# Performance work log

Hardware: AMD Instinct MI355X
Metric: run time of the kernel (lower is better)

Reference implementation:

```python
import jax, jax.numpy as jnp
import numpy as np

B, S, D, H = 2, 2048, 1024, 16
DK = D // H  # 64
ROPE_THETA = 10000.0


def apply_rope(t, positions):
    # t: [B, H, S, DK]; positions: [B, S]
    half = DK // 2
    inv_freq = 1.0 / (ROPE_THETA ** (jnp.arange(0, DK, 2, dtype=jnp.float32) / DK))  # [half]
    ang = positions.astype(jnp.float32)[:, None, :, None] * inv_freq  # [B,1,S,half]
    cos, sin = jnp.cos(ang), jnp.sin(ang)
    t_even = t[..., 0::2]
    t_odd = t[..., 1::2]
    r_even = t_even * cos - t_odd * sin
    r_odd = t_even * sin + t_odd * cos
    # interleave back to original layout
    return jnp.stack([r_even, r_odd], axis=-1).reshape(t.shape)


def setup_inputs() -> dict:
    key = jax.random.key(0)
    ks = jax.random.split(key, 5)
    x = jax.random.normal(ks[0], (B, S, D), dtype=jnp.float32)
    token_positions = jnp.broadcast_to(jnp.arange(S, dtype=jnp.int64 if jax.config.jax_enable_x64 else jnp.int32), (B, S))
    w_q = jax.random.normal(ks[1], (D, D), dtype=jnp.float32)
    w_k = jax.random.normal(ks[2], (D, D), dtype=jnp.float32)
    w_v = jax.random.normal(ks[3], (D, D), dtype=jnp.float32)
    w_o = jax.random.normal(ks[4], (D, D), dtype=jnp.float32)
    return {"x": x, "token_positions": token_positions, "w_q": w_q, "w_k": w_k, "w_v": w_v, "w_o": w_o}


def reference(x, token_positions, w_q, w_k, w_v, w_o):
    # project: weights stored as (h*d_k, d_model)
    wq = w_q.reshape(H, DK, D)
    wk = w_k.reshape(H, DK, D)
    wv = w_v.reshape(H, DK, D)
    q = jnp.einsum('bsd,hkd->bhsk', x, wq)  # [B,H,S,DK]
    k = jnp.einsum('bsd,hkd->bhsk', x, wk)
    v = jnp.einsum('bsd,hkd->bhsk', x, wv)
    q = apply_rope(q, token_positions)
    k = apply_rope(k, token_positions)
    scale = 1.0 / jnp.sqrt(jnp.float32(DK))
    scores = jnp.einsum('bhnk,bhmk->bhnm', q, k) * scale  # [B,H,S,S]
    causal = jnp.tril(jnp.ones((S, S), dtype=bool))
    scores = jnp.where(causal, scores, -jnp.inf)
    attn = jax.nn.softmax(scores, axis=-1)
    out = jnp.einsum('bhnm,bhmv->bhnv', attn, v)  # [B,H,S,DK]
    out = jnp.transpose(out, (0, 2, 1, 3)).reshape(B, S, H * DK)
    return jnp.einsum('bsf,df->bsd', out, w_o)
```

## Files before the change

### kernel.cpp

```cpp
#include <hip/hip_runtime.h>

typedef unsigned short u16;
typedef unsigned int u32;
typedef __attribute__((ext_vector_type(8))) __bf16 bf16x8;
typedef __attribute__((ext_vector_type(4))) float f32x4;

#define NSEQ 2048
#define NDIM 1024
#define NHEAD 16
#define NTOK 4096
#define NX   4194304
#define NWEL 1048576

__device__ __forceinline__ u16 f2bf(float f) {
  unsigned u = __float_as_uint(f);
  return (u16)((u + 0x7fffu + ((u >> 16) & 1u)) >> 16);
}
__device__ __forceinline__ float bf2f(u16 h) {
  return __uint_as_float(((unsigned)h) << 16);
}
__device__ __forceinline__ bf16x8 ld16(const u16* p) {
  int4 v = *reinterpret_cast<const int4*>(p);
  return __builtin_bit_cast(bf16x8, v);
}
__device__ __forceinline__ f32x4 mfma16(bf16x8 a, bf16x8 b, f32x4 c) {
  return __builtin_amdgcn_mfma_f32_16x16x32_bf16(a, b, c, 0, 0, 0);
}
__device__ __forceinline__ u32 cvtpk(float lo, float hi) {
  u32 r;
  asm("v_cvt_pk_bf16_f32 %0, %1, %2" : "=v"(r) : "v"(lo), "v"(hi));
  return r;
}
__device__ __forceinline__ void gload16(const u16* g, u16* l) {
  __builtin_amdgcn_global_load_lds(
      (const __attribute__((address_space(1))) void*)g,
      (__attribute__((address_space(3))) void*)l, 16, 0, 0);
}

#define GEMM_PROLOGUE                                                         \
  const int tid = threadIdx.x;                                                \
  const int lane = tid & 63, wid = tid >> 6;                                  \
  const int wm = wid >> 1, wn = wid & 1;                                      \
  const int lr = lane & 15, lg = lane >> 4;                                   \
  const int srow_ = tid >> 2;                                                 \
  const int sch_ = ((tid & 3) ^ ((tid >> 3) & 3)) * 8;                        \
  const int rsw_ = (lg ^ ((lr >> 1) & 3)) * 8;

#define STAGE3(BB, AH, AL, BH, BL, T0, J0, K0)                                \
  {                                                                           \
    u16* bb_ = (BB);                                                          \
    gload16(AH + (size_t)((T0) + srow_) * NDIM + (K0) + sch_, bb_ + tid * 8); \
    gload16(AH + (size_t)((T0) + 64 + srow_) * NDIM + (K0) + sch_,            \
            bb_ + 2048 + tid * 8);                                            \
    gload16(BH + (size_t)((J0) + srow_) * NDIM + (K0) + sch_,                 \
            bb_ + 4096 + tid * 8);                                            \
    gload16(BH + (size_t)((J0) + 64 + srow_) * NDIM + (K0) + sch_,            \
            bb_ + 6144 + tid * 8);                                            \
    gload16(AL + (size_t)((T0) + srow_) * NDIM + (K0) + sch_,                 \
            bb_ + 8192 + tid * 8);                                            \
    gload16(AL + (size_t)((T0) + 64 + srow_) * NDIM + (K0) + sch_,            \
            bb_ + 10240 + tid * 8);                                           \
    gload16(BL + (size_t)((J0) + srow_) * NDIM + (K0) + sch_,                 \
            bb_ + 12288 + tid * 8);                                           \
    gload16(BL + (size_t)((J0) + 64 + srow_) * NDIM + (K0) + sch_,            \
            bb_ + 14336 + tid * 8);                                           \
  }

#define GEMM3_LOOP(AH, AL, BH, BL, T0, J0)                                    \
  STAGE3(lds, AH, AL, BH, BL, T0, J0, 0)                                      \
  __syncthreads();                                                            \
  for (int k0 = 0; k0 < NDIM; k0 += 32) {                                     \
    u16* cb_ = lds + ((k0 >> 5) & 1) * 16384;                                 \
    if (k0 + 32 < NDIM) {                                                     \
      u16* nb_ = lds + ((((k0 >> 5) & 1) ^ 1) * 16384);                       \
      STAGE3(nb_, AH, AL, BH, BL, T0, J0, k0 + 32)                            \
    }                                                                         \
    bf16x8 afh[4], afl[4];                                                    \
    _Pragma("unroll") for (int m = 0; m < 4; m++) {                           \
      int off = (wm * 64 + m * 16 + lr) * 32 + rsw_;                          \
      afh[m] = ld16(cb_ + off);                                               \
      afl[m] = ld16(cb_ + 8192 + off);                                        \
    }                                                                         \
    _Pragma("unroll") for (int n = 0; n < 4; n++) {                           \
      int off = (wn * 64 + n * 16 + lr) * 32 + rsw_;                          \
      bf16x8 bfh = ld16(cb_ + 4096 + off);                                    \
      bf16x8 bfl = ld16(cb_ + 12288 + off);                                   \
      _Pragma("unroll") for (int m = 0; m < 4; m++) {                         \
        acc[m][n] = mfma16(afh[m], bfh, acc[m][n]);                           \
        acc[m][n] = mfma16(afh[m], bfl, acc[m][n]);                           \
        acc[m][n] = mfma16(afl[m], bfh, acc[m][n]);                           \
      }                                                                       \
    }                                                                         \
    __syncthreads();                                                          \
  }

#define STAGE1(BB, AH, BH, T0, J0, K0)                                        \
  {                                                                           \
    u16* bb_ = (BB);                                                          \
    gload16(AH + (size_t)((T0) + srow_) * NDIM + (K0) + sch_, bb_ + tid * 8); \
    gload16(AH + (size_t)((T0) + 64 + srow_) * NDIM + (K0) + sch_,            \
            bb_ + 2048 + tid * 8);                                            \
    gload16(BH + (size_t)((J0) + srow_) * NDIM + (K0) + sch_,                 \
            bb_ + 4096 + tid * 8);                                            \
    gload16(BH + (size_t)((J0) + 64 + srow_) * NDIM + (K0) + sch_,            \
            bb_ + 6144 + tid * 8);                                            \
  }

#define GEMM1_LOOP(AH, BH, T0, J0)                                            \
  STAGE1(lds, AH, BH, T0, J0, 0)                                              \
  __syncthreads();                                                            \
  for (int k0 = 0; k0 < NDIM; k0 += 32) {                                     \
    u16* cb_ = lds + ((k0 >> 5) & 1) * 8192;                                  \
    if (k0 + 32 < NDIM) {                                                     \
      u16* nb_ = lds + ((((k0 >> 5) & 1) ^ 1) * 8192);                        \
      STAGE1(nb_, AH, BH, T0, J0, k0 + 32)                                    \
    }                                                                         \
    bf16x8 afh[4];                                                            \
    _Pragma("unroll") for (int m = 0; m < 4; m++) {                           \
      int off = (wm * 64 + m * 16 + lr) * 32 + rsw_;                          \
      afh[m] = ld16(cb_ + off);                                               \
    }                                                                         \
    _Pragma("unroll") for (int n = 0; n < 4; n++) {                           \
      int off = (wn * 64 + n * 16 + lr) * 32 + rsw_;                          \
      bf16x8 bfh = ld16(cb_ + 4096 + off);                                    \
      _Pragma("unroll") for (int m = 0; m < 4; m++) {                         \
        acc[m][n] = mfma16(afh[m], bfh, acc[m][n]);                           \
      }                                                                       \
    }                                                                         \
    __syncthreads();                                                          \
  }

__global__ __launch_bounds__(256) void k_prep(
    const float* __restrict__ x, const float* __restrict__ wq,
    const float* __restrict__ wk, const float* __restrict__ wv,
    const float* __restrict__ wo,
    u16* __restrict__ xh, u16* __restrict__ xl,
    u16* __restrict__ wh, u16* __restrict__ wl) {
  int g = blockIdx.x * 256 + threadIdx.x;
  const float4* src;
  u16 *dh, *dl;
  int idx;
  bool wantlo = true;
  if (g < NX / 4) {
    src = (const float4*)x; dh = xh; dl = xl; idx = g;
  } else {
    int z = (g - NX / 4) / (NWEL / 4);
    int r = (g - NX / 4) % (NWEL / 4);
    src = (const float4*)(z == 0 ? wq : z == 1 ? wk : z == 2 ? wv : wo);
    dh = wh + (size_t)z * NWEL; dl = wl + (size_t)z * NWEL; idx = r;
    wantlo = (z < 2);
  }
  float4 v = src[idx];
  u16 h0 = f2bf(v.x), h1 = f2bf(v.y), h2 = f2bf(v.z), h3 = f2bf(v.w);
  ushort4 hv = make_ushort4(h0, h1, h2, h3);
  ((ushort4*)dh)[idx] = hv;
  if (wantlo) {
    ushort4 lv = make_ushort4(f2bf(v.x - bf2f(h0)), f2bf(v.y - bf2f(h1)),
                              f2bf(v.z - bf2f(h2)), f2bf(v.w - bf2f(h3)));
    ((ushort4*)dl)[idx] = lv;
  }
}

__global__ __launch_bounds__(256) void k_tab(float2* __restrict__ csn) {
  int idx = blockIdx.x * 256 + threadIdx.x;
  int p = idx >> 5, j = idx & 31;
  double invf = exp((double)(2 * j) * (-9.210340371976184 / 64.0));
  double ang = (double)p * invf;
  double kq = rint(ang * 0.15915494309189535);
  float a = (float)(ang - kq * 6.283185307179586);
  csn[idx] = make_float2(cosf(a), sinf(a));
}

__global__ __launch_bounds__(256) void k_qkv(
    const u16* __restrict__ xh, const u16* __restrict__ xl,
    const u16* __restrict__ wh, const u16* __restrict__ wl,
    const int* __restrict__ tokpos, const float2* __restrict__ csn,
    u16* __restrict__ qh, u16* __restrict__ ql,
    u16* __restrict__ kh, u16* __restrict__ kl) {
  __shared__ __align__(16) u16 lds[32768];
  const int z = blockIdx.z;
  const int t0 = blockIdx.y * 128, j0 = blockIdx.x * 128;
  const int h0 = j0 >> 6;
  GEMM_PROLOGUE
  const u16* Bh = wh + (size_t)z * NWEL;
  const u16* Bl = wl + (size_t)z * NWEL;
  f32x4 acc[4][4];
#pragma unroll
  for (int m = 0; m < 4; m++)
#pragma unroll
    for (int n = 0; n < 4; n++) acc[m][n] = f32x4{0.f, 0.f, 0.f, 0.f};
  GEMM3_LOOP(xh, xl, Bh, Bl, t0, j0)

  const int b = t0 >> 11, s0 = t0 & 2047;
  u16* dh = (z == 0) ? qh : kh;
  u16* dl = (z == 0) ? ql : kl;
  float rv[4][4][4];
#pragma unroll
  for (int m = 0; m < 4; m++) {
#pragma unroll
    for (int r = 0; r < 4; r++) {
      int pos = tokpos[t0 + wm * 64 + m * 16 + lg * 4 + r];
#pragma unroll
      for (int n = 0; n < 4; n++) {
        float val = acc[m][n][r];
        float nb = __shfl_xor(val, 1);
        int dk = (wn * 64 + n * 16 + lr) & 63;
        float2 cs = csn[pos * 32 + (dk >> 1)];
        rv[m][r][n] = (dk & 1) ? (nb * cs.y + val * cs.x)
                               : (val * cs.x - nb * cs.y);
      }
    }
  }
#pragma unroll
  for (int pass = 0; pass < 2; pass++) {
    __syncthreads();
#pragma unroll
    for (int m = 0; m < 4; m++)
#pragma unroll
      for (int r = 0; r < 4; r++) {
        int rloc = wm * 64 + m * 16 + lg * 4 + r;
#pragma unroll
        for (int n = 0; n < 4; n++) {
          int cloc = wn * 64 + n * 16 + lr;
          float v = rv[m][r][n];
          u16 hi = f2bf(v);
          lds[rloc * 128 + cloc] = pass == 0 ? hi : f2bf(v - bf2f(hi));
        }
      }
    __syncthreads();
    u16* dst = pass == 0 ? dh : dl;
#pragma unroll
    for (int i = 0; i < 8; i++) {
      int idx = tid + i * 256;
      int r = idx >> 4, cc = idx & 15;
      int4 v = *(int4*)(lds + r * 128 + cc * 8);
      int h2 = cc >> 3, dk = (cc & 7) * 8;
      size_t off = ((size_t)((b * NHEAD + h0 + h2) * NSEQ + s0 + r)) * 64 + dk;
      *(int4*)(dst + off) = v;
    }
  }
}

__global__ __launch_bounds__(256) void k_v(
    const u16* __restrict__ xh, const u16* __restrict__ wvh,
    u16* __restrict__ vt) {
  __shared__ __align__(16) u16 lds[16384];
  const int t0 = blockIdx.y * 128, j0 = blockIdx.x * 128;
  const int h0 = j0 >> 6;
  GEMM_PROLOGUE
  f32x4 acc[4][4];
#pragma unroll
  for (int m = 0; m < 4; m++)
#pragma unroll
    for (int n = 0; n < 4; n++) acc[m][n] = f32x4{0.f, 0.f, 0.f, 0.f};
  GEMM1_LOOP(xh, wvh, t0, j0)
  const int b = t0 >> 11, s0 = t0 & 2047;
#pragma unroll
  for (int m = 0; m < 4; m++)
#pragma unroll
    for (int r = 0; r < 4; r++) {
      int rloc = wm * 64 + m * 16 + lg * 4 + r;
#pragma unroll
      for (int n = 0; n < 4; n++) {
        int cloc = wn * 64 + n * 16 + lr;
        lds[cloc * 128 + (rloc ^ ((cloc & 15) << 3))] = f2bf(acc[m][n][r]);
      }
    }
  __syncthreads();
#pragma unroll
  for (int i = 0; i < 8; i++) {
    int idx = tid + i * 256;
    int col = idx >> 4, rc = idx & 15;
    int4 v = *(int4*)(lds + col * 128 + ((rc * 8) ^ ((col & 15) << 3)));
    int h2 = col >> 6, dk = col & 63;
    size_t off = ((size_t)((b * NHEAD + h0 + h2) * 64 + dk)) * NSEQ + s0 + rc * 8;
    *(int4*)(vt + off) = v;
  }
}

#define ATT_STAGE(SEL, KT)                                                    \
  _Pragma("unroll") for (int j_ = 0; j_ < 6; j_++) {                          \
    int seg_ = w * 6 + j_;                                                    \
    int ten_ = seg_ >> 3, sub_ = seg_ & 7;                                    \
    int row_ = sub_ * 8 + (lane >> 3);                                        \
    int sc_ = ((lane & 7) * 8) ^ ((row_ & 7) * 8);             \
    u16* dst_ = (ten_ == 0 ? &skh[SEL][0]                                     \
                           : ten_ == 1 ? &skl[SEL][0] : &svb[SEL][0]) +       \
                sub_ * 512;                                                   \
    const u16* src_ =                                                         \
        (ten_ == 2)                                                           \
            ? vt + vbase + (size_t)row_ * NSEQ + (KT) * 64 + sc_              \
            : (ten_ == 0 ? kh : kl) + base + (size_t)((KT) * 64 + row_) * 64 + sc_; \
    gload16(src_, dst_);                                                      \
  }

__global__ __launch_bounds__(256) void k_attn(
    const u16* __restrict__ qh, const u16* __restrict__ ql,
    const u16* __restrict__ kh, const u16* __restrict__ kl,
    const u16* __restrict__ vt, u16* __restrict__ ah) {
  __shared__ __align__(16) u16 skh[2][4096];
  __shared__ __align__(16) u16 skl[2][4096];
  __shared__ __align__(16) u16 svb[2][4096];
  __shared__ __align__(16) u16 sp[4096];
  const int tid = threadIdx.x, lane = tid & 63, w = tid >> 6;
  const int lr = lane & 15, lg = lane >> 4;
  const int fid = blockIdx.y * 16 + blockIdx.x;
  const int vb_ = (fid & 7) * 64 + (fid >> 3);
  const int bh = vb_ >> 4;
  const int qpair = vb_ & 15;
  const size_t base = (size_t)bh * NSEQ * 64;
  const size_t vbase = (size_t)bh * 64 * NSEQ;
  const int b = bh >> 4, h = bh & 15;
  const int qbA = 31 - qpair, qbB = qpair;
  const float SC2 = 0.18033688011112042f;

  for (int ph = 0; ph < 2; ph++) {
    const int qblk = ph ? qbB : qbA;
    const int q0 = qblk * 64;
    const int nt = qblk + 1;
    const int qrow_g = q0 + w * 16 + lr;
    bf16x8 qfh[2], qfl[2];
#pragma unroll
    for (int kk = 0; kk < 2; kk++) {
      qfh[kk] = ld16(qh + base + (size_t)qrow_g * 64 + kk * 32 + lg * 8);
      qfl[kk] = ld16(ql + base + (size_t)qrow_g * 64 + kk * 32 + lg * 8);
    }
    float mrun = -__builtin_inff(), lrun = 0.f;
    f32x4 oacc[4];
#pragma unroll
    for (int nf = 0; nf < 4; nf++) oacc[nf] = f32x4{0.f, 0.f, 0.f, 0.f};

    int sel = 0;
    ATT_STAGE(0, 0)
    __syncthreads();
    for (int kt = 0; kt < nt; kt++) {
      if (kt + 1 < nt) { ATT_STAGE(sel ^ 1, kt + 1) }
      f32x4 sacc[4];
#pragma unroll
      for (int nf = 0; nf < 4; nf++) sacc[nf] = f32x4{0.f, 0.f, 0.f, 0.f};
      __builtin_amdgcn_s_setprio(1);
#pragma unroll
      for (int nf = 0; nf < 4; nf++) {
        int krow = nf * 16 + lr;
        int swz = (krow & 7) * 8;
#pragma unroll
        for (int kk = 0; kk < 2; kk++) {
          int off = krow * 64 + ((kk * 32 + lg * 8) ^ swz);
          bf16x8 kfh = ld16(&skh[sel][0] + off);
          bf16x8 kfl = ld16(&skl[sel][0] + off);
          sacc[nf] = mfma16(kfh, qfh[kk], sacc[nf]);
          sacc[nf] = mfma16(kfl, qfh[kk], sacc[nf]);
          sacc[nf] = mfma16(kfh, qfl[kk], sacc[nf]);
        }
      }
      __builtin_amdgcn_s_setprio(0);
      float sv[4][4], mm[4];
#pragma unroll
      for (int nf = 0; nf < 4; nf++) {
#pragma unroll
        for (int r = 0; r < 4; r++) sv[nf][r] = sacc[nf][r] * SC2;
      }
      if (kt == qblk) {
#pragma unroll
        for (int nf = 0; nf < 4; nf++)
#pragma unroll
          for (int r = 0; r < 4; r++) {
            int colg = kt * 64 + nf * 16 + lg * 4 + r;
            if (colg > qrow_g) sv[nf][r] = -__builtin_inff();
          }
      }
#pragma unroll
      for (int nf = 0; nf < 4; nf++)
        mm[nf] = fmaxf(fmaxf(sv[nf][0], sv[nf][1]), fmaxf(sv[nf][2], sv[nf][3]));
      float rmax = fmaxf(fmaxf(mm[0], mm[1]), fmaxf(mm[2], mm[3]));
      rmax = fmaxf(rmax, __shfl_xor(rmax, 16));
      rmax = fmaxf(rmax, __shfl_xor(rmax, 32));
      float alpha = 1.f;
      bool resc = __any(rmax > mrun + 8.f);
      if (resc) {
        float mnew = fmaxf(mrun, rmax);
        alpha = exp2f(mrun - mnew);
        mrun = mnew;
        lrun *= alpha;
      }
      float p[4][4];
      float ss[4];
#pragma unroll
      for (int nf = 0; nf < 4; nf++) {
#pragma unroll
        for (int r = 0; r < 4; r++) p[nf][r] = exp2f(sv[nf][r] - mrun);
        ss[nf] = (p[nf][0] + p[nf][1]) + (p[nf][2] + p[nf][3]);
      }
      float rsum = (ss[0] + ss[1]) + (ss[2] + ss[3]);
      rsum += __shfl_xor(rsum, 16);
      rsum += __shfl_xor(rsum, 32);
      lrun += rsum;
      {
        int prow = w * 16 + lr;
        int swz = (prow & 7) * 8;
#pragma unroll
        for (int nf = 0; nf < 4; nf++) {
          u32 w0 = cvtpk(p[nf][0], p[nf][1]);
          u32 w1 = cvtpk(p[nf][2], p[nf][3]);
          int col = (nf * 16 + lg * 4) ^ swz;
          *(uint2*)(&sp[prow * 64 + col]) = make_uint2(w0, w1);
        }
      }
      if (resc) {
        float af0 = __shfl(alpha, lg * 4 + 0);
        float af1 = __shfl(alpha, lg * 4 + 1);
        float af2 = __shfl(alpha, lg * 4 + 2);
        float af3 = __shfl(alpha, lg * 4 + 3);
#pragma unroll
        for (int nf = 0; nf < 4; nf++) {
          oacc[nf][0] *= af0; oacc[nf][1] *= af1;
          oacc[nf][2] *= af2; oacc[nf][3] *= af3;
        }
      }
      {
        int prow = w * 16 + lr;
        int pswz = (prow & 7) * 8;
        __builtin_amdgcn_s_setprio(1);
#pragma unroll
        for (int kk = 0; kk < 2; kk++) {
          bf16x8 pa = ld16(&sp[prow * 64 + ((kk * 32 + lg * 8) ^ pswz)]);
#pragma unroll
          for (int nf = 0; nf < 4; nf++) {
            int vrow = nf * 16 + lr;
            bf16x8 vb2 = ld16(&svb[sel][0] + vrow * 64 +
                              ((kk * 32 + lg * 8) ^ ((vrow & 7) * 8)));
            oacc[nf] = mfma16(pa, vb2, oacc[nf]);
          }
        }
        __builtin_amdgcn_s_setprio(0);
      }
      __syncthreads();
      sel ^= 1;
    }
    float inv = 1.0f / lrun;
    float iv0 = __shfl(inv, lg * 4 + 0);
    float iv1 = __shfl(inv, lg * 4 + 1);
    float iv2 = __shfl(inv, lg * 4 + 2);
    float iv3 = __shfl(inv, lg * 4 + 3);
#pragma unroll
    for (int r = 0; r < 4; r++) {
      float ivr = r == 0 ? iv0 : r == 1 ? iv1 : r == 2 ? iv2 : iv3;
      int row = q0 + w * 16 + lg * 4 + r;
      size_t toff = ((size_t)(b * NSEQ + row)) * NDIM + h * 64;
#pragma unroll
      for (int nf = 0; nf < 4; nf++) {
        ah[toff + nf * 16 + lr] = f2bf(oacc[nf][r] * ivr);
      }
    }
  }
}

__global__ __launch_bounds__(256) void k_out(
    const u16* __restrict__ ah, const u16* __restrict__ wh,
    float* __restrict__ out) {
  __shared__ __align__(16) u16 lds[16384];
  const int t0 = blockIdx.y * 128, j0 = blockIdx.x * 128;
  GEMM_PROLOGUE
  f32x4 acc[4][4];
#pragma unroll
  for (int m = 0; m < 4; m++)
#pragma unroll
    for (int n = 0; n < 4; n++) acc[m][n] = f32x4{0.f, 0.f, 0.f, 0.f};
  GEMM1_LOOP(ah, wh, t0, j0)
#pragma unroll
  for (int m = 0; m < 4; m++)
#pragma unroll
    for (int r = 0; r < 4; r++) {
      int row = t0 + wm * 64 + m * 16 + lg * 4 + r;
#pragma unroll
      for (int n = 0; n < 4; n++) {
        int col = j0 + wn * 64 + n * 16 + lr;
        out[(size_t)row * NDIM + col] = acc[m][n][r];
      }
    }
}

extern "C" void kernel_launch(void* const* d_in, const int* in_sizes, int n_in,
                              void* d_out, int out_size, void* d_ws, size_t ws_size,
                              hipStream_t stream) {
  (void)in_sizes; (void)n_in; (void)out_size; (void)ws_size;
  const float* x = (const float*)d_in[0];
  const int* tokpos = (const int*)d_in[1];
  const float* wq = (const float*)d_in[2];
  const float* wk = (const float*)d_in[3];
  const float* wv = (const float*)d_in[4];
  const float* wo = (const float*)d_in[5];
  float* out = (float*)d_out;

  u16* ws = (u16*)d_ws;
  u16* xh = ws;
  u16* xl = xh + NX;
  u16* wh = xl + NX;
  u16* wl = wh + 4 * (size_t)NWEL;
  u16* qh = wl + 4 * (size_t)NWEL;
  u16* ql = qh + NX;
  u16* kh = ql + NX;
  u16* kl = kh + NX;
  u16* vt = kl + NX;
  float2* csn = (float2*)(vt + NX);

  k_prep<<<dim3(8192), dim3(256), 0, stream>>>(x, wq, wk, wv, wo, xh, xl, wh, wl);
  k_tab<<<dim3(256), dim3(256), 0, stream>>>(csn);
  k_qkv<<<dim3(8, 32, 2), dim3(256), 0, stream>>>(xh, xl, wh, wl, tokpos, csn,
                                                  qh, ql, kh, kl);
  k_v<<<dim3(8, 32), dim3(256), 0, stream>>>(xh, wh + 2 * (size_t)NWEL, vt);
  k_attn<<<dim3(16, 32), dim3(256), 0, stream>>>(qh, ql, kh, kl, vt, xh);
  k_out<<<dim3(8, 32), dim3(256), 0, stream>>>(xh, wh + 3 * (size_t)NWEL, out);
}
```

Baseline: 179.7 us.

## Keep P in registers via transposed PV MFMA and one q-tile per block

The attention kernel now computes the output transposed (V·Pᵀ) so the probability fragment can be assembled from registers with lane shuffles instead of round-tripping through a shared-memory P buffer. The sp LDS array and its writes/reads are removed, and rescaling by alpha becomes a per-lane scalar multiply. The grid also changes from paired causal q-tiles per block (long+short) to one q-tile per block with twice as many blocks, which drops the manual load balancing in favour of more parallelism. The shuffles add cross-lane traffic, and the output store is now vectorised per row.

```diff
diff --git a/kernel.cpp b/kernel.cpp
--- a/kernel.cpp
+++ b/kernel.cpp
@@ -301,157 +301,139 @@
   __shared__ __align__(16) u16 skh[2][4096];
   __shared__ __align__(16) u16 skl[2][4096];
   __shared__ __align__(16) u16 svb[2][4096];
-  __shared__ __align__(16) u16 sp[4096];
   const int tid = threadIdx.x, lane = tid & 63, w = tid >> 6;
   const int lr = lane & 15, lg = lane >> 4;
-  const int fid = blockIdx.y * 16 + blockIdx.x;
-  const int vb_ = (fid & 7) * 64 + (fid >> 3);
-  const int bh = vb_ >> 4;
-  const int qpair = vb_ & 15;
+  const int fid = blockIdx.y * 32 + blockIdx.x;
+  const int vb_ = (fid & 7) * 128 + (fid >> 3);
+  const int bh = vb_ >> 5;
+  const int qt = 31 - (vb_ & 31);
   const size_t base = (size_t)bh * NSEQ * 64;
   const size_t vbase = (size_t)bh * 64 * NSEQ;
   const int b = bh >> 4, h = bh & 15;
-  const int qbA = 31 - qpair, qbB = qpair;
+  const int q0 = qt * 64, nt = qt + 1;
   const float SC2 = 0.18033688011112042f;
 
-  for (int ph = 0; ph < 2; ph++) {
-    const int qblk = ph ? qbB : qbA;
-    const int q0 = qblk * 64;
-    const int nt = qblk + 1;
-    const int qrow_g = q0 + w * 16 + lr;
-    bf16x8 qfh[2], qfl[2];
-#pragma unroll
-    for (int kk = 0; kk < 2; kk++) {
-      qfh[kk] = ld16(qh + base + (size_t)qrow_g * 64 + kk * 32 + lg * 8);
-      qfl[kk] = ld16(ql + base + (size_t)qrow_g * 64 + kk * 32 + lg * 8);
-    }
-    float mrun = -__builtin_inff(), lrun = 0.f;
-    f32x4 oacc[4];
-#pragma unroll
-    for (int nf = 0; nf < 4; nf++) oacc[nf] = f32x4{0.f, 0.f, 0.f, 0.f};
-
-    int sel = 0;
-    ATT_STAGE(0, 0)
+  const int qrow_g = q0 + w * 16 + lr;
+  bf16x8 qfh[2], qfl[2];
+#pragma unroll
+  for (int kk = 0; kk < 2; kk++) {
+    qfh[kk] = ld16(qh + base + (size_t)qrow_g * 64 + kk * 32 + lg * 8);
+    qfl[kk] = ld16(ql + base + (size_t)qrow_g * 64 + kk * 32 + lg * 8);
+  }
+  float mrun = -__builtin_inff(), lrun = 0.f;
+  f32x4 oaccT[4];
+#pragma unroll
+  for (int d = 0; d < 4; d++) oaccT[d] = f32x4{0.f, 0.f, 0.f, 0.f};
+
+  int sel = 0;
+  ATT_STAGE(0, 0)
+  __syncthreads();
+  for (int kt = 0; kt < nt; kt++) {
+    if (kt + 1 < nt) { ATT_STAGE(sel ^ 1, kt + 1) }
+    f32x4 sacc[4];
+#pragma unroll
+    for (int nf = 0; nf < 4; nf++) sacc[nf] = f32x4{0.f, 0.f, 0.f, 0.f};
+    __builtin_amdgcn_s_setprio(1);
+#pragma unroll
+    for (int nf = 0; nf < 4; nf++) {
+      int krow = nf * 16 + lr;
+      int swz = (krow & 7) * 8;
+#pragma unroll
+      for (int kk = 0; kk < 2; kk++) {
+        int off = krow * 64 + ((kk * 32 + lg * 8) ^ swz);
+        bf16x8 kfh = ld16(&skh[sel][0] + off);
+        bf16x8 kfl = ld16(&skl[sel][0] + off);
+        sacc[nf] = mfma16(kfh, qfh[kk], sacc[nf]);
+        sacc[nf] = mfma16(kfl, qfh[kk], sacc[nf]);
+        sacc[nf] = mfma16(kfh, qfl[kk], sacc[nf]);
+      }
+    }
+    __builtin_amdgcn_s_setprio(0);
+    float sv[4][4], mm[4];
+#pragma unroll
+    for (int nf = 0; nf < 4; nf++) {
+#pragma unroll
+      for (int r = 0; r < 4; r++) sv[nf][r] = sacc[nf][r] * SC2;
+    }
+    if (kt == qt) {
+#pragma unroll
+      for (int nf = 0; nf < 4; nf++)
+#pragma unroll
+        for (int r = 0; r < 4; r++) {
+          int colg = kt * 64 + nf * 16 + lg * 4 + r;
+          if (colg > qrow_g) sv[nf][r] = -__builtin_inff();
+        }
+    }
+#pragma unroll
+    for (int nf = 0; nf < 4; nf++)
+      mm[nf] = fmaxf(fmaxf(sv[nf][0], sv[nf][1]), fmaxf(sv[nf][2], sv[nf][3]));
+    float rmax = fmaxf(fmaxf(mm[0], mm[1]), fmaxf(mm[2], mm[3]));
+    rmax = fmaxf(rmax, __shfl_xor(rmax, 16));
+    rmax = fmaxf(rmax, __shfl_xor(rmax, 32));
+    bool resc = __any(rmax > mrun + 8.f);
+    if (resc) {
+      float mnew = fmaxf(mrun, rmax);
+      float alpha = exp2f(mrun - mnew);
+      mrun = mnew;
+      lrun *= alpha;
+#pragma unroll
+      for (int d = 0; d < 4; d++) oaccT[d] = oaccT[d] * alpha;
+    }
+    float p[4][4], ss[4];
+#pragma unroll
+    for (int nf = 0; nf < 4; nf++) {
+#pragma unroll
+      for (int r = 0; r < 4; r++) p[nf][r] = exp2f(sv[nf][r] - mrun);
+      ss[nf] = (p[nf][0] + p[nf][1]) + (p[nf][2] + p[nf][3]);
+    }
+    float rsum = (ss[0] + ss[1]) + (ss[2] + ss[3]);
+    rsum += __shfl_xor(rsum, 16);
+    rsum += __shfl_xor(rsum, 32);
+    lrun += rsum;
+    u32 pw0[4], pw1[4];
+#pragma unroll
+    for (int nf = 0; nf < 4; nf++) {
+      pw0[nf] = cvtpk(p[nf][0], p[nf][1]);
+      pw1[nf] = cvtpk(p[nf][2], p[nf][3]);
+    }
+    {
+      const int slo = ((lg & 1) << 5) + lr;
+      const int shi = slo + 16;
+      const bool hisel = (lg & 2) != 0;
+      __builtin_amdgcn_s_setprio(1);
+#pragma unroll
+      for (int kk = 0; kk < 2; kk++) {
+        u32 a0 = (u32)__shfl((int)pw0[kk * 2], slo);
+        u32 b0 = (u32)__shfl((int)pw0[kk * 2 + 1], slo);
+        u32 a1 = (u32)__shfl((int)pw1[kk * 2], slo);
+        u32 b1 = (u32)__shfl((int)pw1[kk * 2 + 1], slo);
+        u32 a2 = (u32)__shfl((int)pw0[kk * 2], shi);
+        u32 b2 = (u32)__shfl((int)pw0[kk * 2 + 1], shi);
+        u32 a3 = (u32)__shfl((int)pw1[kk * 2], shi);
+        u32 b3 = (u32)__shfl((int)pw1[kk * 2 + 1], shi);
+        uint4 pwv = make_uint4(hisel ? b0 : a0, hisel ? b1 : a1,
+                               hisel ? b2 : a2, hisel ? b3 : a3);
+        bf16x8 pfrag = __builtin_bit_cast(bf16x8, pwv);
+#pragma unroll
+        for (int dblk = 0; dblk < 4; dblk++) {
+          int row = dblk * 16 + lr;
+          bf16x8 vfrag = ld16(&svb[sel][0] + row * 64 +
+                              ((kk * 32 + lg * 8) ^ ((row & 7) * 8)));
+          oaccT[dblk] = mfma16(vfrag, pfrag, oaccT[dblk]);
+        }
+      }
+      __builtin_amdgcn_s_setprio(0);
+    }
     __syncthreads();
-    for (int kt = 0; kt < nt; kt++) {
-      if (kt + 1 < nt) { ATT_STAGE(sel ^ 1, kt + 1) }
-      f32x4 sacc[4];
-#pragma unroll
-      for (int nf = 0; nf < 4; nf++) sacc[nf] = f32x4{0.f, 0.f, 0.f, 0.f};
-      __builtin_amdgcn_s_setprio(1);
-#pragma unroll
-      for (int nf = 0; nf < 4; nf++) {
-        int krow = nf * 16 + lr;
-        int swz = (krow & 7) * 8;
-#pragma unroll
-        for (int kk = 0; kk < 2; kk++) {
-          int off = krow * 64 + ((kk * 32 + lg * 8) ^ swz);
-          bf16x8 kfh = ld16(&skh[sel][0] + off);
-          bf16x8 kfl = ld16(&skl[sel][0] + off);
-          sacc[nf] = mfma16(kfh, qfh[kk], sacc[nf]);
-          sacc[nf] = mfma16(kfl, qfh[kk], sacc[nf]);
-          sacc[nf] = mfma16(kfh, qfl[kk], sacc[nf]);
-        }
-      }
-      __builtin_amdgcn_s_setprio(0);
-      float sv[4][4], mm[4];
-#pragma unroll
-      for (int nf = 0; nf < 4; nf++) {
-#pragma unroll
-        for (int r = 0; r < 4; r++) sv[nf][r] = sacc[nf][r] * SC2;
-      }
-      if (kt == qblk) {
-#pragma unroll
-        for (int nf = 0; nf < 4; nf++)
-#pragma unroll
-          for (int r = 0; r < 4; r++) {
-            int colg = kt * 64 + nf * 16 + lg * 4 + r;
-            if (colg > qrow_g) sv[nf][r] = -__builtin_inff();
-          }
-      }
-#pragma unroll
-      for (int nf = 0; nf < 4; nf++)
-        mm[nf] = fmaxf(fmaxf(sv[nf][0], sv[nf][1]), fmaxf(sv[nf][2], sv[nf][3]));
-      float rmax = fmaxf(fmaxf(mm[0], mm[1]), fmaxf(mm[2], mm[3]));
-      rmax = fmaxf(rmax, __shfl_xor(rmax, 16));
-      rmax = fmaxf(rmax, __shfl_xor(rmax, 32));
-      float alpha = 1.f;
-      bool resc = __any(rmax > mrun + 8.f);
-      if (resc) {
-        float mnew = fmaxf(mrun, rmax);
-        alpha = exp2f(mrun - mnew);
-        mrun = mnew;
-        lrun *= alpha;
-      }
-      float p[4][4];
-      float ss[4];
-#pragma unroll
-      for (int nf = 0; nf < 4; nf++) {
-#pragma unroll
-        for (int r = 0; r < 4; r++) p[nf][r] = exp2f(sv[nf][r] - mrun);
-        ss[nf] = (p[nf][0] + p[nf][1]) + (p[nf][2] + p[nf][3]);
-      }
-      float rsum = (ss[0] + ss[1]) + (ss[2] + ss[3]);
-      rsum += __shfl_xor(rsum, 16);
-      rsum += __shfl_xor(rsum, 32);
-      lrun += rsum;
-      {
-        int prow = w * 16 + lr;
-        int swz = (prow & 7) * 8;
-#pragma unroll
-        for (int nf = 0; nf < 4; nf++) {
-          u32 w0 = cvtpk(p[nf][0], p[nf][1]);
-          u32 w1 = cvtpk(p[nf][2], p[nf][3]);
-          int col = (nf * 16 + lg * 4) ^ swz;
-          *(uint2*)(&sp[prow * 64 + col]) = make_uint2(w0, w1);
-        }
-      }
-      if (resc) {
-        float af0 = __shfl(alpha, lg * 4 + 0);
-        float af1 = __shfl(alpha, lg * 4 + 1);
-        float af2 = __shfl(alpha, lg * 4 + 2);
-        float af3 = __shfl(alpha, lg * 4 + 3);
-#pragma unroll
-        for (int nf = 0; nf < 4; nf++) {
-          oacc[nf][0] *= af0; oacc[nf][1] *= af1;
-          oacc[nf][2] *= af2; oacc[nf][3] *= af3;
-        }
-      }
-      {
-        int prow = w * 16 + lr;
-        int pswz = (prow & 7) * 8;
-        __builtin_amdgcn_s_setprio(1);
-#pragma unroll
-        for (int kk = 0; kk < 2; kk++) {
-          bf16x8 pa = ld16(&sp[prow * 64 + ((kk * 32 + lg * 8) ^ pswz)]);
-#pragma unroll
-          for (int nf = 0; nf < 4; nf++) {
-            int vrow = nf * 16 + lr;
-            bf16x8 vb2 = ld16(&svb[sel][0] + vrow * 64 +
-                              ((kk * 32 + lg * 8) ^ ((vrow & 7) * 8)));
-            oacc[nf] = mfma16(pa, vb2, oacc[nf]);
-          }
-        }
-        __builtin_amdgcn_s_setprio(0);
-      }
-      __syncthreads();
-      sel ^= 1;
-    }
-    float inv = 1.0f / lrun;
-    float iv0 = __shfl(inv, lg * 4 + 0);
-    float iv1 = __shfl(inv, lg * 4 + 1);
-    float iv2 = __shfl(inv, lg * 4 + 2);
-    float iv3 = __shfl(inv, lg * 4 + 3);
-#pragma unroll
-    for (int r = 0; r < 4; r++) {
-      float ivr = r == 0 ? iv0 : r == 1 ? iv1 : r == 2 ? iv2 : iv3;
-      int row = q0 + w * 16 + lg * 4 + r;
-      size_t toff = ((size_t)(b * NSEQ + row)) * NDIM + h * 64;
-#pragma unroll
-      for (int nf = 0; nf < 4; nf++) {
-        ah[toff + nf * 16 + lr] = f2bf(oacc[nf][r] * ivr);
-      }
-    }
+    sel ^= 1;
+  }
+  float inv = 1.0f / lrun;
+  size_t toff = ((size_t)(b * NSEQ + qrow_g)) * NDIM + h * 64 + lg * 4;
+#pragma unroll
+  for (int dblk = 0; dblk < 4; dblk++) {
+    u32 w0 = cvtpk(oaccT[dblk][0] * inv, oaccT[dblk][1] * inv);
+    u32 w1 = cvtpk(oaccT[dblk][2] * inv, oaccT[dblk][3] * inv);
+    *(uint2*)(ah + toff + dblk * 16) = make_uint2(w0, w1);
   }
 }
 
@@ -509,6 +491,6 @@
   k_qkv<<<dim3(8, 32, 2), dim3(256), 0, stream>>>(xh, xl, wh, wl, tokpos, csn,
                                                   qh, ql, kh, kl);
   k_v<<<dim3(8, 32), dim3(256), 0, stream>>>(xh, wh + 2 * (size_t)NWEL, vt);
-  k_attn<<<dim3(16, 32), dim3(256), 0, stream>>>(qh, ql, kh, kl, vt, xh);
+  k_attn<<<dim3(32, 32), dim3(256), 0, stream>>>(qh, ql, kh, kl, vt, xh);
   k_out<<<dim3(8, 32), dim3(256), 0, stream>>>(xh, wh + 3 * (size_t)NWEL, out);
 }
```

Result: slower. 205.6 us (+14.4%).
